# Performance work log

Measured on AMD Instinct MI355X. Metric: run time of the kernel, lower is better.

The kernel has to match this reference:

```python
import jax, jax.numpy as jnp
import numpy as np

EPS = 1e-7  # keras.backend.epsilon()
CANONICAL_SIZE = 224.0
CANONICAL_LEVEL = 1.0
MIN_LEVEL, MAX_LEVEL = 0, 4


def _crop_and_resize(feat, boxes, crop_h, crop_w):
    """TF crop_and_resize (bilinear, extrapolation_value=0) for one image.
    feat: [H, W, C]; boxes: [N, 4] normalized (y1, x1, y2, x2).
    Returns [N, crop_h, crop_w, C]."""
    H, W, C = feat.shape
    hf = jnp.asarray(H - 1, feat.dtype)
    wf = jnp.asarray(W - 1, feat.dtype)
    y1, x1, y2, x2 = boxes[:, 0], boxes[:, 1], boxes[:, 2], boxes[:, 3]
    ty = jnp.arange(crop_h, dtype=feat.dtype) / (crop_h - 1)  # [ch]
    tx = jnp.arange(crop_w, dtype=feat.dtype) / (crop_w - 1)  # [cw]
    ys = (y1[:, None] + (y2 - y1)[:, None] * ty[None, :]) * hf  # [N, ch]
    xs = (x1[:, None] + (x2 - x1)[:, None] * tx[None, :]) * wf  # [N, cw]
    valid_y = (ys >= 0) & (ys <= hf)
    valid_x = (xs >= 0) & (xs <= wf)
    y0 = jnp.floor(ys)
    x0 = jnp.floor(xs)
    ly = ys - y0  # lerp weights [N, ch]
    lx = xs - x0  # [N, cw]
    y0i = jnp.clip(y0, 0, H - 1).astype(jnp.int32)
    y1i = jnp.clip(y0 + 1, 0, H - 1).astype(jnp.int32)
    x0i = jnp.clip(x0, 0, W - 1).astype(jnp.int32)
    x1i = jnp.clip(x0 + 1, 0, W - 1).astype(jnp.int32)
    # gather 4 corners -> [N, ch, cw, C]
    f00 = feat[y0i[:, :, None], x0i[:, None, :]]
    f01 = feat[y0i[:, :, None], x1i[:, None, :]]
    f10 = feat[y1i[:, :, None], x0i[:, None, :]]
    f11 = feat[y1i[:, :, None], x1i[:, None, :]]
    wy = ly[:, :, None, None]
    wx = lx[:, None, :, None]
    top = f00 + (f01 - f00) * wx
    bot = f10 + (f11 - f10) * wx
    out = top + (bot - top) * wy
    valid = (valid_y[:, :, None] & valid_x[:, None, :])[..., None]
    return jnp.where(valid, out, jnp.zeros((), feat.dtype))


def _map_to_level(boxes):
    w = boxes[:, 2] - boxes[:, 0]
    h = boxes[:, 3] - boxes[:, 1]
    size = jnp.sqrt(w * h)
    levels = jnp.floor(CANONICAL_LEVEL + jnp.log2(size / CANONICAL_SIZE + EPS))
    return jnp.clip(levels, MIN_LEVEL, MAX_LEVEL).astype(jnp.int32)


def roi_align(detections, fpn, top_k=1000, crop_size=(14, 14)):
    det = detections[0]                       # [N, 4+num_classes]
    scores = jnp.max(det[:, 4:], axis=1)      # [N]
    _, idx = jax.lax.top_k(scores, top_k)
    det = det[idx]                            # [K, 4+nc]
    levels = _map_to_level(det[:, :4])        # [K]
    # original concatenates level-0 rois, then level-1, ... == stable sort by level
    order = jnp.argsort(levels, stable=True)
    det = det[order]
    levels = levels[order]
    ch, cw = crop_size
    C = fpn[0].shape[-1]
    out = jnp.zeros((top_k, ch, cw, C), fpn[0].dtype)
    for i, f in enumerate(fpn):
        feat = f[0]                           # [H, W, C]
        H, W = feat.shape[0], feat.shape[1]
        hf = jnp.asarray(H - 1, feat.dtype)
        wf = jnp.asarray(W - 1, feat.dtype)
        boxes = jnp.stack([det[:, 1] / hf, det[:, 0] / wf,
                           det[:, 3] / hf, det[:, 2] / wf], axis=1)
        crops = _crop_and_resize(feat, boxes, ch, cw)
        out = jnp.where((levels == i)[:, None, None, None], crops, out)
    return out[None]                          # [1, K, ch, cw, C]


def setup_inputs() -> dict:
    key = jax.random.key(0)
    ks = jax.random.split(key, 10)
    N, NC = 5000, 80
    cx = jax.random.uniform(ks[0], (N,)) * 1024.0
    cy = jax.random.uniform(ks[1], (N,)) * 1024.0
    size = jnp.exp2(jax.random.uniform(ks[2], (N,)) * 5.0 + 5.0)   # 32..1024
    ar = jnp.exp2(jax.random.uniform(ks[3], (N,)) * 2.0 - 1.0)     # 0.5..2
    w = size * jnp.sqrt(ar)
    h = size / jnp.sqrt(ar)
    x1 = jnp.maximum(cx - w / 2, 0.0)
    y1 = jnp.maximum(cy - h / 2, 0.0)
    x2 = x1 + w
    y2 = y1 + h
    cls = jax.random.uniform(ks[4], (N, NC))
    detections = jnp.concatenate(
        [jnp.stack([x1, y1, x2, y2], axis=1), cls], axis=1)[None]  # [1,N,84]
    C = 256
    shapes = [256, 128, 64, 32, 16]
    fpn = {f"p{i}": jax.random.normal(ks[5 + i], (1, s, s, C), jnp.float32)
           for i, s in enumerate(shapes)}
    return {"detections": detections, **fpn}


def reference(detections, p0, p1, p2, p3, p4):
    return roi_align(detections, [p0, p1, p2, p3, p4],
                     top_k=1000, crop_size=(14, 14))
```

## Files before the change

### kernel.cpp

```cpp
#include <hip/hip_runtime.h>

#define NDET 5000
#define NCLS 80
#define DSTR 84
#define TOPK 1000
#define CROP 14
#define NPIX (CROP * CROP)
#define C    256

#define JCHUNK 250
#define ICHUNK 256

typedef float v4f __attribute__((ext_vector_type(4)));

__global__ void scores_kernel(const float* __restrict__ det, float* __restrict__ scores,
                              int* __restrict__ rank) {
    int i = blockIdx.x * blockDim.x + threadIdx.x;
    if (i >= NDET) return;
    const float* row = det + i * DSTR + 4;
    float m = row[0];
    #pragma unroll
    for (int c = 1; c < NCLS; ++c) m = fmaxf(m, row[c]);
    scores[i] = m;
    rank[i] = 0;
}

__global__ __launch_bounds__(ICHUNK) void rank_kernel(const float* __restrict__ scores,
                                                      int* __restrict__ rank) {
    __shared__ float s[JCHUNK];
    int jbase = blockIdx.y * JCHUNK;
    for (int t = threadIdx.x; t < JCHUNK; t += blockDim.x) s[t] = scores[jbase + t];
    __syncthreads();
    int i = blockIdx.x * ICHUNK + threadIdx.x;
    if (i >= NDET) return;
    float my = scores[i];
    int r = 0;
    #pragma unroll 5
    for (int t = 0; t < JCHUNK; ++t) {
        float v = s[t];
        int j = jbase + t;
        r += (v > my) | ((v == my) & (j < i));
    }
    atomicAdd(&rank[i], r);
}

__global__ __launch_bounds__(1024) void order_kernel(const float* __restrict__ det,
                                                     const int* __restrict__ rank,
                                                     int* __restrict__ slot_det,
                                                     int* __restrict__ slot_level) {
    __shared__ int topk_idx_s[TOPK];
    __shared__ unsigned long long wave_tot[16];
    int r = threadIdx.x;
    for (int i = r; i < NDET; i += 1024) {
        int rk = rank[i];
        if (rk < TOPK) topk_idx_s[rk] = i;
    }
    __syncthreads();

    int di = 0, L = 0;
    unsigned long long key = 0;
    if (r < TOPK) {
        di = topk_idx_s[r];
        const float* b = det + di * DSTR;
        float w = b[2] - b[0];
        float h = b[3] - b[1];
        float sz = sqrtf(w * h);
        float lf = floorf(1.0f + log2f(sz / 224.0f + 1e-7f));
        lf = fminf(fmaxf(lf, 0.0f), 4.0f);
        L = (int)lf;
        key = 1ULL << (12 * L);
    }
    unsigned long long incl = key;
    #pragma unroll
    for (int d = 1; d < 64; d <<= 1) {
        unsigned long long up = __shfl_up(incl, d, 64);
        if ((r & 63) >= d) incl += up;
    }
    int wave = r >> 6;
    if ((r & 63) == 63) wave_tot[wave] = incl;
    __syncthreads();
    unsigned long long waveoff = 0, total = 0;
    for (int w = 0; w < 16; ++w) {
        unsigned long long t = wave_tot[w];
        if (w < wave) waveoff += t;
        total += t;
    }
    if (r < TOPK) {
        unsigned long long excl = waveoff + incl - key;
        int base = 0;
        for (int l = 0; l < L; ++l) base += (int)((total >> (12 * l)) & 0xFFF);
        int within = (int)((excl >> (12 * L)) & 0xFFF);
        int pos = base + within;
        slot_det[pos] = di;
        slot_level[pos] = L;
    }
}

__global__ __launch_bounds__(256) void crop_kernel(
    const float* __restrict__ det,
    const float* __restrict__ p0, const float* __restrict__ p1,
    const float* __restrict__ p2, const float* __restrict__ p3,
    const float* __restrict__ p4,
    const int* __restrict__ slot_det, const int* __restrict__ slot_level,
    float* __restrict__ out)
{
    int wave = threadIdx.x >> 6;
    int lane = threadIdx.x & 63;
    int slot = blockIdx.x / 13;
    int sub  = blockIdx.x % 13;
    int pbase = sub * 16 + wave * 4;

    int di = slot_det[slot];
    int L  = slot_level[slot];

    const float* feat; int H;
    switch (L) {
        case 0:  feat = p0; H = 256; break;
        case 1:  feat = p1; H = 128; break;
        case 2:  feat = p2; H = 64;  break;
        case 3:  feat = p3; H = 32;  break;
        default: feat = p4; H = 16;  break;
    }
    float hf = (float)(H - 1);

    const float* b = det + di * DSTR;
    float x1n = b[0] / hf, y1n = b[1] / hf;
    float x2n = b[2] / hf, y2n = b[3] / hf;
    float* outbase = out + (size_t)slot * NPIX * C;

    #pragma unroll
    for (int j = 0; j < 4; ++j) {
        int p = pbase + j;
        if (p >= NPIX) break;
        int py = p / CROP;
        int px = p - py * CROP;
        float ty = (float)py / 13.0f;
        float tx = (float)px / 13.0f;
        float ys = (y1n + (y2n - y1n) * ty) * hf;
        float xs = (x1n + (x2n - x1n) * tx) * hf;

        v4f* outp = (v4f*)(outbase + (size_t)p * C) + lane;

        bool valid = (ys >= 0.0f) & (ys <= hf) & (xs >= 0.0f) & (xs <= hf);
        if (!valid) {
            v4f z = {0.0f, 0.0f, 0.0f, 0.0f};
            *outp = z;
            continue;
        }

        float y0f = floorf(ys), x0f = floorf(xs);
        float ly = ys - y0f,    lx = xs - x0f;
        int y0i = (int)fminf(fmaxf(y0f,        0.0f), hf);
        int y1i = (int)fminf(fmaxf(y0f + 1.0f, 0.0f), hf);
        int x0i = (int)fminf(fmaxf(x0f,        0.0f), hf);
        int x1i = (int)fminf(fmaxf(x0f + 1.0f, 0.0f), hf);

        v4f f00 = ((const v4f*)(feat + (size_t)(y0i * H + x0i) * C))[lane];
        v4f f01 = ((const v4f*)(feat + (size_t)(y0i * H + x1i) * C))[lane];
        v4f f10 = ((const v4f*)(feat + (size_t)(y1i * H + x0i) * C))[lane];
        v4f f11 = ((const v4f*)(feat + (size_t)(y1i * H + x1i) * C))[lane];

        v4f top = f00 + (f01 - f00) * lx;
        v4f bot = f10 + (f11 - f10) * lx;
        v4f o   = top + (bot - top) * ly;
        *outp = o;
    }
}

extern "C" void kernel_launch(void* const* d_in, const int* in_sizes, int n_in,
                              void* d_out, int out_size, void* d_ws, size_t ws_size,
                              hipStream_t stream) {
    const float* det = (const float*)d_in[0];
    const float* p0  = (const float*)d_in[1];
    const float* p1  = (const float*)d_in[2];
    const float* p2  = (const float*)d_in[3];
    const float* p3  = (const float*)d_in[4];
    const float* p4  = (const float*)d_in[5];
    float* out = (float*)d_out;

    char* ws = (char*)d_ws;
    float* scores    = (float*)(ws + 0);
    int*   rank      = (int*)(ws + 20000);
    int*   slot_det  = (int*)(ws + 40000);
    int*   slot_lvl  = (int*)(ws + 44000);

    scores_kernel<<<(NDET + 255) / 256, 256, 0, stream>>>(det, scores, rank);
    dim3 rg((NDET + ICHUNK - 1) / ICHUNK, NDET / JCHUNK);
    rank_kernel<<<rg, ICHUNK, 0, stream>>>(scores, rank);
    order_kernel<<<1, 1024, 0, stream>>>(det, rank, slot_det, slot_lvl);
    crop_kernel<<<TOPK * 13, 256, 0, stream>>>(det, p0, p1, p2, p3, p4,
                                               slot_det, slot_lvl, out);
}
```

Baseline: 290.5 us.

## Precompute per-slot box params and use one pixel per wave in crop kernel

```diff
diff --git a/kernel.cpp b/kernel.cpp
--- a/kernel.cpp
+++ b/kernel.cpp
@@ -14,15 +14,26 @@
 typedef float v4f __attribute__((ext_vector_type(4)));
 
 __global__ void scores_kernel(const float* __restrict__ det, float* __restrict__ scores,
-                              int* __restrict__ rank) {
+                              int* __restrict__ rank, int* __restrict__ lvl_all) {
     int i = blockIdx.x * blockDim.x + threadIdx.x;
     if (i >= NDET) return;
-    const float* row = det + i * DSTR + 4;
-    float m = row[0];
+    const float* row = det + i * DSTR;
+    const v4f* cls = (const v4f*)(row + 4);
+    v4f m4 = cls[0];
     #pragma unroll
-    for (int c = 1; c < NCLS; ++c) m = fmaxf(m, row[c]);
-    scores[i] = m;
+    for (int c = 1; c < NCLS / 4; ++c) {
+        v4f v = cls[c];
+        m4.x = fmaxf(m4.x, v.x); m4.y = fmaxf(m4.y, v.y);
+        m4.z = fmaxf(m4.z, v.z); m4.w = fmaxf(m4.w, v.w);
+    }
+    scores[i] = fmaxf(fmaxf(m4.x, m4.y), fmaxf(m4.z, m4.w));
     rank[i] = 0;
+    float w = row[2] - row[0];
+    float h = row[3] - row[1];
+    float sz = sqrtf(w * h);
+    float lf = floorf(1.0f + log2f(sz / 224.0f + 1e-7f));
+    lf = fminf(fmaxf(lf, 0.0f), 4.0f);
+    lvl_all[i] = (int)lf;
 }
 
 __global__ __launch_bounds__(ICHUNK) void rank_kernel(const float* __restrict__ scores,
@@ -46,7 +57,8 @@
 
 __global__ __launch_bounds__(1024) void order_kernel(const float* __restrict__ det,
                                                      const int* __restrict__ rank,
-                                                     int* __restrict__ slot_det,
+                                                     const int* __restrict__ lvl_all,
+                                                     v4f* __restrict__ slot_params,
                                                      int* __restrict__ slot_level) {
     __shared__ int topk_idx_s[TOPK];
     __shared__ unsigned long long wave_tot[16];
@@ -61,13 +73,7 @@
     unsigned long long key = 0;
     if (r < TOPK) {
         di = topk_idx_s[r];
-        const float* b = det + di * DSTR;
-        float w = b[2] - b[0];
-        float h = b[3] - b[1];
-        float sz = sqrtf(w * h);
-        float lf = floorf(1.0f + log2f(sz / 224.0f + 1e-7f));
-        lf = fminf(fmaxf(lf, 0.0f), 4.0f);
-        L = (int)lf;
+        L = lvl_all[di];
         key = 1ULL << (12 * L);
     }
     unsigned long long incl = key;
@@ -91,80 +97,73 @@
         for (int l = 0; l < L; ++l) base += (int)((total >> (12 * l)) & 0xFFF);
         int within = (int)((excl >> (12 * L)) & 0xFFF);
         int pos = base + within;
-        slot_det[pos] = di;
+        int H = 256 >> L;
+        float hf = (float)(H - 1);
+        const float* b = det + di * DSTR;
+        float x1n = b[0] / hf, y1n = b[1] / hf;
+        float x2n = b[2] / hf, y2n = b[3] / hf;
+        v4f prm = {x1n, y1n, x2n - x1n, y2n - y1n};
+        slot_params[pos] = prm;
         slot_level[pos] = L;
     }
 }
 
 __global__ __launch_bounds__(256) void crop_kernel(
-    const float* __restrict__ det,
     const float* __restrict__ p0, const float* __restrict__ p1,
     const float* __restrict__ p2, const float* __restrict__ p3,
     const float* __restrict__ p4,
-    const int* __restrict__ slot_det, const int* __restrict__ slot_level,
+    const v4f* __restrict__ slot_params, const int* __restrict__ slot_level,
     float* __restrict__ out)
 {
     int wave = threadIdx.x >> 6;
     int lane = threadIdx.x & 63;
-    int slot = blockIdx.x / 13;
-    int sub  = blockIdx.x % 13;
-    int pbase = sub * 16 + wave * 4;
+    int slot = blockIdx.x / 49;
+    int p    = (blockIdx.x % 49) * 4 + wave;
+    int py = p / CROP, px = p - py * CROP;
 
-    int di = slot_det[slot];
-    int L  = slot_level[slot];
-
-    const float* feat; int H;
+    int L = slot_level[slot];
+    const float* feat;
     switch (L) {
-        case 0:  feat = p0; H = 256; break;
-        case 1:  feat = p1; H = 128; break;
-        case 2:  feat = p2; H = 64;  break;
-        case 3:  feat = p3; H = 32;  break;
-        default: feat = p4; H = 16;  break;
+        case 0:  feat = p0; break;
+        case 1:  feat = p1; break;
+        case 2:  feat = p2; break;
+        case 3:  feat = p3; break;
+        default: feat = p4; break;
     }
+    int H = 256 >> L;
     float hf = (float)(H - 1);
 
-    const float* b = det + di * DSTR;
-    float x1n = b[0] / hf, y1n = b[1] / hf;
-    float x2n = b[2] / hf, y2n = b[3] / hf;
-    float* outbase = out + (size_t)slot * NPIX * C;
+    v4f prm = slot_params[slot];
+    float ty = (float)py / 13.0f;
+    float tx = (float)px / 13.0f;
+    float ys = (prm.y + prm.w * ty) * hf;
+    float xs = (prm.x + prm.z * tx) * hf;
 
-    #pragma unroll
-    for (int j = 0; j < 4; ++j) {
-        int p = pbase + j;
-        if (p >= NPIX) break;
-        int py = p / CROP;
-        int px = p - py * CROP;
-        float ty = (float)py / 13.0f;
-        float tx = (float)px / 13.0f;
-        float ys = (y1n + (y2n - y1n) * ty) * hf;
-        float xs = (x1n + (x2n - x1n) * tx) * hf;
+    v4f* outp = (v4f*)(out + (size_t)(slot * NPIX + p) * C) + lane;
 
-        v4f* outp = (v4f*)(outbase + (size_t)p * C) + lane;
+    bool valid = (ys >= 0.0f) & (ys <= hf) & (xs >= 0.0f) & (xs <= hf);
+    if (!valid) {
+        v4f z = {0.0f, 0.0f, 0.0f, 0.0f};
+        *outp = z;
+        return;
+    }
 
-        bool valid = (ys >= 0.0f) & (ys <= hf) & (xs >= 0.0f) & (xs <= hf);
-        if (!valid) {
-            v4f z = {0.0f, 0.0f, 0.0f, 0.0f};
-            *outp = z;
-            continue;
-        }
+    float y0f = floorf(ys), x0f = floorf(xs);
+    float ly = ys - y0f,    lx = xs - x0f;
+    int y0i = (int)fminf(fmaxf(y0f,        0.0f), hf);
+    int y1i = (int)fminf(fmaxf(y0f + 1.0f, 0.0f), hf);
+    int x0i = (int)fminf(fmaxf(x0f,        0.0f), hf);
+    int x1i = (int)fminf(fmaxf(x0f + 1.0f, 0.0f), hf);
 
-        float y0f = floorf(ys), x0f = floorf(xs);
-        float ly = ys - y0f,    lx = xs - x0f;
-        int y0i = (int)fminf(fmaxf(y0f,        0.0f), hf);
-        int y1i = (int)fminf(fmaxf(y0f + 1.0f, 0.0f), hf);
-        int x0i = (int)fminf(fmaxf(x0f,        0.0f), hf);
-        int x1i = (int)fminf(fmaxf(x0f + 1.0f, 0.0f), hf);
+    v4f f00 = ((const v4f*)(feat + (size_t)(y0i * H + x0i) * C))[lane];
+    v4f f01 = ((const v4f*)(feat + (size_t)(y0i * H + x1i) * C))[lane];
+    v4f f10 = ((const v4f*)(feat + (size_t)(y1i * H + x0i) * C))[lane];
+    v4f f11 = ((const v4f*)(feat + (size_t)(y1i * H + x1i) * C))[lane];
 
-        v4f f00 = ((const v4f*)(feat + (size_t)(y0i * H + x0i) * C))[lane];
-        v4f f01 = ((const v4f*)(feat + (size_t)(y0i * H + x1i) * C))[lane];
-        v4f f10 = ((const v4f*)(feat + (size_t)(y1i * H + x0i) * C))[lane];
-        v4f f11 = ((const v4f*)(feat + (size_t)(y1i * H + x1i) * C))[lane];
-
-        v4f top = f00 + (f01 - f00) * lx;
-        v4f bot = f10 + (f11 - f10) * lx;
-        v4f o   = top + (bot - top) * ly;
-        *outp = o;
-    }
+    v4f top = f00 + (f01 - f00) * lx;
+    v4f bot = f10 + (f11 - f10) * lx;
+    v4f o   = top + (bot - top) * ly;
+    *outp = o;
 }
 
 extern "C" void kernel_launch(void* const* d_in, const int* in_sizes, int n_in,
@@ -179,15 +178,16 @@
     float* out = (float*)d_out;
 
     char* ws = (char*)d_ws;
-    float* scores    = (float*)(ws + 0);
-    int*   rank      = (int*)(ws + 20000);
-    int*   slot_det  = (int*)(ws + 40000);
-    int*   slot_lvl  = (int*)(ws + 44000);
+    float* scores      = (float*)(ws + 0);
+    int*   rank        = (int*)(ws + 20000);
+    int*   lvl_all     = (int*)(ws + 40000);
+    v4f*   slot_params = (v4f*)(ws + 60000);
+    int*   slot_lvl    = (int*)(ws + 76000);
 
-    scores_kernel<<<(NDET + 255) / 256, 256, 0, stream>>>(det, scores, rank);
+    scores_kernel<<<(NDET + 255) / 256, 256, 0, stream>>>(det, scores, rank, lvl_all);
     dim3 rg((NDET + ICHUNK - 1) / ICHUNK, NDET / JCHUNK);
     rank_kernel<<<rg, ICHUNK, 0, stream>>>(scores, rank);
-    order_kernel<<<1, 1024, 0, stream>>>(det, rank, slot_det, slot_lvl);
-    crop_kernel<<<TOPK * 13, 256, 0, stream>>>(det, p0, p1, p2, p3, p4,
-                                               slot_det, slot_lvl, out);
+    order_kernel<<<1, 1024, 0, stream>>>(det, rank, lvl_all, slot_params, slot_lvl);
+    crop_kernel<<<TOPK * 49, 256, 0, stream>>>(p0, p1, p2, p3, p4,
+                                               slot_params, slot_lvl, out);
 }
```

Measured after the change: 281.6 us. 3.1% less time.
